# Performance work log

Measured on AMD Instinct MI355X. Metric: run time of the kernel, lower is better.

Reference implementation:

```python
import jax, jax.numpy as jnp
import numpy as np

B, S, D = 2, 2048, 2048
H, KV, DK = 16, 4, 128
G = H // KV  # GQA groups
EPS = 1e-6
BASE = 10000.0


def _rope_tables(seq_len, dim):
    inv_freq = 1.0 / (BASE ** (jnp.arange(0, dim, 2, dtype=jnp.float32) / dim))
    t = jnp.arange(seq_len, dtype=jnp.float32)
    freqs = t[:, None] * inv_freq[None, :]            # [S, dim/2]
    emb = jnp.concatenate([freqs, freqs], axis=-1)    # [S, dim]
    # broadcast over [b, s, h, d]
    return jnp.cos(emb)[None, :, None, :], jnp.sin(emb)[None, :, None, :]


def _rotate_half(x):
    x1, x2 = jnp.split(x, 2, axis=-1)
    return jnp.concatenate([-x2, x1], axis=-1)


def _rms_norm(x, w):
    return x * jax.lax.rsqrt(jnp.mean(x * x, axis=-1, keepdims=True) + EPS) * w


def setup_inputs() -> dict:
    key = jax.random.key(0)
    ks = jax.random.split(key, 5)
    std = 0.02
    return {
        "x": jax.random.normal(ks[0], (B, S, D), jnp.float32),
        "Wq": jax.random.normal(ks[1], (D, H * DK), jnp.float32) * std,
        "Wk": jax.random.normal(ks[2], (D, KV * DK), jnp.float32) * std,
        "Wv": jax.random.normal(ks[3], (D, KV * DK), jnp.float32) * std,
        "Wo": jax.random.normal(ks[4], (H * DK, D), jnp.float32) * std,
        "q_norm_w": jnp.ones((DK,), jnp.float32),
        "k_norm_w": jnp.ones((DK,), jnp.float32),
    }


def reference(x, Wq, Wk, Wv, Wo, q_norm_w, k_norm_w):
    b, s, d = x.shape
    q = (x @ Wq).reshape(b, s, H, DK)
    k = (x @ Wk).reshape(b, s, KV, DK)
    v = (x @ Wv).reshape(b, s, KV, DK)

    # per-head RMSNorm on q/k
    q = _rms_norm(q, q_norm_w)
    k = _rms_norm(k, k_norm_w)

    # RoPE (applied in [b, s, h, d] layout like the original)
    cos, sin = _rope_tables(s, DK)
    q = q * cos + _rotate_half(q) * sin
    k = k * cos + _rotate_half(k) * sin

    # GQA attention without materializing repeated K/V:
    # q: [b, kv, g, s, d];  k, v: [b, kv, s, d]
    q = q.transpose(0, 2, 1, 3).reshape(b, KV, G, s, DK)
    k = k.transpose(0, 2, 1, 3)
    v = v.transpose(0, 2, 1, 3)

    scale = 1.0 / np.sqrt(DK)
    scores = jnp.einsum('bkgqd,bkpd->bkgqp', q, k) * scale  # [b,kv,g,s,s]
    causal = jnp.tril(jnp.ones((s, s), dtype=bool))
    scores = jnp.where(causal, scores, jnp.finfo(scores.dtype).min)
    attn = jax.nn.softmax(scores, axis=-1)
    out = jnp.einsum('bkgqp,bkpd->bkgqd', attn, v)           # [b,kv,g,s,d]

    out = out.reshape(b, H, s, DK).transpose(0, 2, 1, 3).reshape(b, s, H * DK)
    return out @ Wo
```

## Files before the change

kernel.cpp:

```cpp
#include <hip/hip_runtime.h>

typedef __attribute__((ext_vector_type(4))) float f32x4;
typedef __attribute__((ext_vector_type(8))) short s16x8;

struct alignas(8) us4 { ushort x, y, z, w; };

__device__ __forceinline__ ushort f2bf(float f) {
  unsigned u = __builtin_bit_cast(unsigned, f);
  u += 0x7fffu + ((u >> 16) & 1u);
  return (ushort)(u >> 16);
}
__device__ __forceinline__ float bf2f(ushort h) {
  unsigned u = ((unsigned)h) << 16;
  return __builtin_bit_cast(float, u);
}

__device__ __forceinline__ void gload_lds16(const ushort* g, ushort* l) {
  __builtin_amdgcn_global_load_lds((const __attribute__((address_space(1))) unsigned int*)g,
                                   (__attribute__((address_space(3))) unsigned int*)l, 16, 0, 0);
}

__global__ __launch_bounds__(256) void preproc_kernel(
    const float* __restrict__ x, const float* __restrict__ Wq, const float* __restrict__ Wk,
    const float* __restrict__ Wv, const float* __restrict__ Wo,
    ushort* __restrict__ xb, ushort* __restrict__ WqkvT, ushort* __restrict__ WoT,
    float* __restrict__ rc, float* __restrict__ rs) {
  __shared__ float tile[32][33];
  int bid = blockIdx.x, tid = threadIdx.x;
  if (bid < 2048) {
    const int n4 = 4096 * 2048 / 4;
    for (int i = bid * 256 + tid; i < n4; i += 2048 * 256) {
      float4 v = reinterpret_cast<const float4*>(x)[i];
      us4 o;
      o.x = f2bf(v.x); o.y = f2bf(v.y); o.z = f2bf(v.z); o.w = f2bf(v.w);
      reinterpret_cast<us4*>(xb)[i] = o;
    }
  } else if (bid < 2560) {
    int t = (bid - 2048) * 4 + (tid >> 6), j = tid & 63;
    float inv = expf(-(float)j * (9.210340371976184f / 64.0f));
    float ang = (float)t * inv;
    float s, c;
    sincosf(ang, &s, &c);
    rc[t * 64 + j] = c;
    rs[t * 64 + j] = s;
  } else {
    int wid = bid - 2560;
    const float* src;
    ushort* dst;
    int C, bx, by;
    if (wid < 4096) { src = Wq; dst = WqkvT; C = 2048; bx = wid & 63; by = wid >> 6; }
    else if (wid < 5120) { int w2 = wid - 4096; src = Wk; dst = WqkvT + (size_t)2048 * 2048; C = 512; bx = w2 & 15; by = w2 >> 4; }
    else if (wid < 6144) { int w2 = wid - 5120; src = Wv; dst = WqkvT + (size_t)2560 * 2048; C = 512; bx = w2 & 15; by = w2 >> 4; }
    else { int w2 = wid - 6144; src = Wo; dst = WoT; C = 2048; bx = w2 & 63; by = w2 >> 6; }
    int c0 = bx * 32, r0 = by * 32;
    int tx = tid & 31, ty = tid >> 5;
#pragma unroll
    for (int i = 0; i < 4; ++i)
      tile[ty + i * 8][tx] = src[(size_t)(r0 + ty + i * 8) * C + c0 + tx];
    __syncthreads();
#pragma unroll
    for (int i = 0; i < 4; ++i)
      dst[(size_t)(c0 + ty + i * 8) * 2048 + r0 + tx] = f2bf(tile[tx][ty + i * 8]);
  }
}

__global__ __launch_bounds__(256) void postqkv_kernel(
    const ushort* __restrict__ qkv, const float* __restrict__ kw,
    ushort* __restrict__ Kb, ushort* __restrict__ vt,
    const float* __restrict__ rc, const float* __restrict__ rs) {
  __shared__ ushort tile[64][136];
  int bid = blockIdx.x, tid = threadIdx.x;
  if (bid < 4096) {
    int wv = tid >> 6, lane = tid & 63;
    int row = bid * 4 + wv;
    int token = row >> 2, head = row & 3;
    const ushort* p = qkv + (size_t)token * 3072 + 2048 + head * 128;
    float x1 = bf2f(p[lane]), x2 = bf2f(p[lane + 64]);
    float ss = x1 * x1 + x2 * x2;
#pragma unroll
    for (int m = 32; m > 0; m >>= 1) ss += __shfl_xor(ss, m);
    float r = rsqrtf(ss * (1.0f / 128.0f) + 1e-6f);
    float xn1 = x1 * r * kw[lane], xn2 = x2 * r * kw[lane + 64];
    int t = token & 2047;
    float c = rc[t * 64 + lane], s = rs[t * 64 + lane];
    ushort* o = Kb + (size_t)token * 512 + head * 128;
    o[lane] = f2bf(xn1 * c - xn2 * s);
    o[lane + 64] = f2bf(xn2 * c + xn1 * s);
  } else {
    int bx = bid - 4096;
    int st = bx & 31, kvh = (bx >> 5) & 3, b = bx >> 7;
    int s0 = st * 64;
#pragma unroll
    for (int p = 0; p < 4; ++p) {
      int idx = p * 2048 + tid * 8;
      int s = idx >> 7, d = idx & 127;
      *(s16x8*)&tile[s][d] =
          *(const s16x8*)&qkv[(size_t)(b * 2048 + s0 + s) * 3072 + 2560 + kvh * 128 + d];
    }
    __syncthreads();
#pragma unroll
    for (int p = 0; p < 4; ++p) {
      int idx = p * 2048 + tid * 8;
      int d = idx >> 6, s = idx & 63;
      s16x8 v;
#pragma unroll
      for (int u = 0; u < 8; ++u) v[u] = (short)tile[s + u][d];
      *(s16x8*)&vt[(size_t)((b * 4 + kvh) * 128 + d) * 2048 + s0 + s] = v;
    }
  }
}

template <bool OUTF32>
__global__ __launch_bounds__(512, 2) void gemm256_kernel(const ushort* __restrict__ A,
                                                         const ushort* __restrict__ Bt,
                                                         void* __restrict__ Cp,
                                                         int M, int N, int K) {
  __shared__ ushort As[3][256][64];
  __shared__ ushort Bs[3][128][64];
  int tid = threadIdx.x;
  int lane = tid & 63, wv = tid >> 6;
  int wm = wv >> 1, wn = wv & 1;
  int lr = lane & 15, lg = lane >> 4;
  int nwg = gridDim.x * gridDim.y;
  int flat = blockIdx.y * gridDim.x + blockIdx.x;
  int swz = (flat & 7) * (nwg >> 3) + (flat >> 3);
  int bx = swz % gridDim.x, by = swz / gridDim.x;
  int m0 = by * 256, n0 = bx * 128;
  int srow8 = lane >> 3;
  int gcol = ((lane & 7) * 8) ^ (srow8 << 3);
  int nt = K >> 6;

  const ushort* Abase = A + (size_t)m0 * K;
  const ushort* Bbase = Bt + (size_t)n0 * K;

  auto stageA = [&](int slot, int t, int p) {
    int r0 = (wv * 4 + p) * 8;
    gload_lds16(&Abase[(size_t)(r0 + srow8) * K + t * 64 + gcol], &As[slot][r0][0]);
  };
  auto stageB = [&](int slot, int t, int p) {
    int r0 = (wv * 2 + p) * 8;
    gload_lds16(&Bbase[(size_t)(r0 + srow8) * K + t * 64 + gcol], &Bs[slot][r0][0]);
  };

  stageA(0, 0, 0); stageA(0, 0, 1); stageB(0, 0, 0);
  stageA(0, 0, 2); stageA(0, 0, 3); stageB(0, 0, 1);
  stageA(1, 1, 0); stageA(1, 1, 1); stageB(1, 1, 0);
  stageA(1, 1, 2); stageA(1, 1, 3); stageB(1, 1, 1);

  f32x4 acc[4][4] = {};
  int arow[4], brow[4], aswz[4], bswz[4];
#pragma unroll
  for (int i = 0; i < 4; ++i) {
    arow[i] = wm * 64 + i * 16 + lr;
    aswz[i] = (arow[i] & 7) << 3;
    brow[i] = wn * 64 + i * 16 + lr;
    bswz[i] = (brow[i] & 7) << 3;
  }

  for (int t = 0; t < nt; ++t) {
    int cur = t % 3, pf = (t + 2) % 3;
    if (t + 1 < nt) {
      asm volatile("s_waitcnt vmcnt(6)" ::: "memory");
    } else {
      asm volatile("s_waitcnt vmcnt(0)" ::: "memory");
    }
    __builtin_amdgcn_s_barrier();
    bool do_pf = (t + 2) < nt;
    {
      s16x8 a[4], b[4];
#pragma unroll
      for (int i = 0; i < 4; ++i) a[i] = *(const s16x8*)&As[cur][arow[i]][(lg * 8) ^ aswz[i]];
#pragma unroll
      for (int j = 0; j < 4; ++j) b[j] = *(const s16x8*)&Bs[cur][brow[j]][(lg * 8) ^ bswz[j]];
      if (do_pf) { stageA(pf, t + 2, 0); stageA(pf, t + 2, 1); stageB(pf, t + 2, 0); }
      __builtin_amdgcn_s_setprio(1);
#pragma unroll
      for (int i = 0; i < 4; ++i)
#pragma unroll
        for (int j = 0; j < 4; ++j)
          acc[i][j] = __builtin_amdgcn_mfma_f32_16x16x32_bf16(a[i], b[j], acc[i][j], 0, 0, 0);
      __builtin_amdgcn_s_setprio(0);
    }
    {
      s16x8 a[4], b[4];
#pragma unroll
      for (int i = 0; i < 4; ++i) a[i] = *(const s16x8*)&As[cur][arow[i]][(32 + lg * 8) ^ aswz[i]];
#pragma unroll
      for (int j = 0; j < 4; ++j) b[j] = *(const s16x8*)&Bs[cur][brow[j]][(32 + lg * 8) ^ bswz[j]];
      if (do_pf) { stageA(pf, t + 2, 2); stageA(pf, t + 2, 3); stageB(pf, t + 2, 1); }
      __builtin_amdgcn_s_setprio(1);
#pragma unroll
      for (int i = 0; i < 4; ++i)
#pragma unroll
        for (int j = 0; j < 4; ++j)
          acc[i][j] = __builtin_amdgcn_mfma_f32_16x16x32_bf16(a[i], b[j], acc[i][j], 0, 0, 0);
      __builtin_amdgcn_s_setprio(0);
    }
  }
#pragma unroll
  for (int i = 0; i < 4; ++i)
#pragma unroll
    for (int j = 0; j < 4; ++j) {
      int row = m0 + wm * 64 + i * 16 + lg * 4;
      int col = n0 + wn * 64 + j * 16 + lr;
#pragma unroll
      for (int r = 0; r < 4; ++r) {
        float v = acc[i][j][r];
        if (OUTF32)
          reinterpret_cast<float*>(Cp)[(size_t)(row + r) * N + col] = v;
        else
          reinterpret_cast<ushort*>(Cp)[(size_t)(row + r) * N + col] = f2bf(v);
      }
    }
}

__global__ __launch_bounds__(256, 2) void attn_kernel(const ushort* __restrict__ QKV,
                                                      const ushort* __restrict__ Kn,
                                                      const ushort* __restrict__ Vt,
                                                      ushort* __restrict__ AO,
                                                      const float* __restrict__ rc,
                                                      const float* __restrict__ rs,
                                                      const float* __restrict__ qw) {
  __shared__ ushort Ks[2][64][128];
  __shared__ ushort Vs[2][128][64];
  __shared__ ushort Ps[4][32][64];
  int bxi = blockIdx.x;
  int g = bxi >> 5, bh = bxi & 31;
  int qt = (g < 8) ? (15 - g) : (g - 8);
  int b = bh >> 4, h = bh & 15, kvh = h >> 2;
  int q0 = qt * 128;
  int nt = 2 * qt + 2;
  int tid = threadIdx.x, lane = tid & 63, w = tid >> 6;
  int lr = lane & 15, lg = lane >> 4;

  int ksrow = lane >> 4, kscol = (lane & 15) * 8;
  int vsrow = lane >> 3, vscol = (lane & 7) * 8;

  auto stage = [&](int c, int t) {
    int p0 = t * 64;
#pragma unroll
    for (int p = 0; p < 4; ++p) {
      int r0 = w * 16 + p * 4;
      int row = r0 + ksrow;
      int gc = kscol ^ ((row & 7) << 3);
      gload_lds16(&Kn[(size_t)(b * 2048 + p0 + row) * 512 + kvh * 128 + gc], &Ks[c][r0][0]);
    }
#pragma unroll
    for (int p = 0; p < 4; ++p) {
      int r0 = w * 32 + p * 8;
      int row = r0 + vsrow;
      int gc = vscol ^ ((row & 7) << 3);
      gload_lds16(&Vt[(size_t)((b * 4 + kvh) * 128 + row) * 2048 + p0 + gc], &Vs[c][r0][0]);
    }
  };

  stage(0, 0);

  const float QSCALE = 0.12751744f;
  s16x8 qf[2][4];
#pragma unroll
  for (int qa = 0; qa < 2; ++qa) {
    int t_tok = q0 + w * 32 + qa * 16 + lr;
    const ushort* qp = QKV + (size_t)(b * 2048 + t_tok) * 3072 + h * 128;
    float xv[4][8];
    float ss = 0.f;
#pragma unroll
    for (int ks = 0; ks < 4; ++ks) {
      s16x8 raw = *(const s16x8*)&qp[ks * 32 + lg * 8];
#pragma unroll
      for (int j = 0; j < 8; ++j) {
        float x = bf2f((ushort)raw[j]);
        xv[ks][j] = x;
        ss += x * x;
      }
    }
    ss += __shfl_xor(ss, 16);
    ss += __shfl_xor(ss, 32);
    float rms = rsqrtf(ss * (1.0f / 128.0f) + 1e-6f);
#pragma unroll
    for (int ks = 0; ks < 2; ++ks) {
      int dbase = ks * 32 + lg * 8;
      float cc[8], sn[8], w1[8], w2[8];
      *(float4*)&cc[0] = *(const float4*)&rc[(size_t)t_tok * 64 + dbase];
      *(float4*)&cc[4] = *(const float4*)&rc[(size_t)t_tok * 64 + dbase + 4];
      *(float4*)&sn[0] = *(const float4*)&rs[(size_t)t_tok * 64 + dbase];
      *(float4*)&sn[4] = *(const float4*)&rs[(size_t)t_tok * 64 + dbase + 4];
      *(float4*)&w1[0] = *(const float4*)&qw[dbase];
      *(float4*)&w1[4] = *(const float4*)&qw[dbase + 4];
      *(float4*)&w2[0] = *(const float4*)&qw[dbase + 64];
      *(float4*)&w2[4] = *(const float4*)&qw[dbase + 68];
      s16x8 o1, o2;
#pragma unroll
      for (int j = 0; j < 8; ++j) {
        float x1 = xv[ks][j] * rms * w1[j];
        float x2 = xv[ks + 2][j] * rms * w2[j];
        o1[j] = (short)f2bf((x1 * cc[j] - x2 * sn[j]) * QSCALE);
        o2[j] = (short)f2bf((x2 * cc[j] + x1 * sn[j]) * QSCALE);
      }
      qf[qa][ks] = o1;
      qf[qa][ks + 2] = o2;
    }
  }

  f32x4 O[2][8] = {};
  float mrow[2] = {-1e30f, -1e30f};
  float lrow[2] = {0.f, 0.f};

  for (int t = 0; t < nt; ++t) {
    int c = t & 1;
    if (t + 1 < nt) {
      stage(c ^ 1, t + 1);
      asm volatile("s_waitcnt vmcnt(8)" ::: "memory");
    } else {
      asm volatile("s_waitcnt vmcnt(0)" ::: "memory");
    }
    __builtin_amdgcn_s_barrier();

    bool skip = (t == 2 * qt + 1) && (w < 2);
    if (!skip) {
      f32x4 sacc[2][4] = {};
      __builtin_amdgcn_s_setprio(1);
#pragma unroll
      for (int ks = 0; ks < 4; ++ks) {
        s16x8 bk[4];
#pragma unroll
        for (int fp = 0; fp < 4; ++fp) {
          int kr = fp * 16 + lr;
          bk[fp] = *(const s16x8*)&Ks[c][kr][(ks * 32 + lg * 8) ^ ((kr & 7) << 3)];
        }
#pragma unroll
        for (int qa = 0; qa < 2; ++qa)
#pragma unroll
          for (int fp = 0; fp < 4; ++fp)
            sacc[qa][fp] = __builtin_amdgcn_mfma_f32_16x16x32_bf16(bk[fp], qf[qa][ks], sacc[qa][fp], 0, 0, 0);
      }
      __builtin_amdgcn_s_setprio(0);

      if (t >= 2 * qt) {
        int p0 = t * 64;
#pragma unroll
        for (int qa = 0; qa < 2; ++qa)
#pragma unroll
          for (int fp = 0; fp < 4; ++fp)
#pragma unroll
            for (int r = 0; r < 4; ++r) {
              int qg = q0 + w * 32 + qa * 16 + lr;
              int pg = p0 + fp * 16 + lg * 4 + r;
              if (pg > qg) sacc[qa][fp][r] = -1e30f;
            }
      }

      float pml[2];
#pragma unroll
      for (int qa = 0; qa < 2; ++qa) {
        float m0 = fmaxf(fmaxf(sacc[qa][0][0], sacc[qa][0][1]), fmaxf(sacc[qa][0][2], sacc[qa][0][3]));
        float m1 = fmaxf(fmaxf(sacc[qa][1][0], sacc[qa][1][1]), fmaxf(sacc[qa][1][2], sacc[qa][1][3]));
        float m2 = fmaxf(fmaxf(sacc[qa][2][0], sacc[qa][2][1]), fmaxf(sacc[qa][2][2], sacc[qa][2][3]));
        float m3 = fmaxf(fmaxf(sacc[qa][3][0], sacc[qa][3][1]), fmaxf(sacc[qa][3][2], sacc[qa][3][3]));
        pml[qa] = fmaxf(fmaxf(m0, m1), fmaxf(m2, m3));
      }
      bool need = (pml[0] > mrow[0] + 8.0f) | (pml[1] > mrow[1] + 8.0f);
      if (__any((int)need)) {
        float fsc[2];
#pragma unroll
        for (int qa = 0; qa < 2; ++qa) {
          float pm = fmaxf(pml[qa], __shfl_xor(pml[qa], 16));
          pm = fmaxf(pm, __shfl_xor(pm, 32));
          float mn = fmaxf(mrow[qa], pm);
          fsc[qa] = __builtin_amdgcn_exp2f(mrow[qa] - mn);
          mrow[qa] = mn;
          lrow[qa] *= fsc[qa];
        }
#pragma unroll
        for (int qa = 0; qa < 2; ++qa) {
          float fo[4];
#pragma unroll
          for (int r = 0; r < 4; ++r) fo[r] = __shfl(fsc[qa], lg * 4 + r);
#pragma unroll
          for (int fn = 0; fn < 8; ++fn)
#pragma unroll
            for (int r = 0; r < 4; ++r) O[qa][fn][r] *= fo[r];
        }
      }
#pragma unroll
      for (int qa = 0; qa < 2; ++qa) {
        float ls = 0.f;
        int prow = qa * 16 + lr;
        int swz = (lr & 7) << 3;
#pragma unroll
        for (int fp = 0; fp < 4; ++fp) {
          float e0 = __builtin_amdgcn_exp2f(sacc[qa][fp][0] - mrow[qa]);
          float e1 = __builtin_amdgcn_exp2f(sacc[qa][fp][1] - mrow[qa]);
          float e2 = __builtin_amdgcn_exp2f(sacc[qa][fp][2] - mrow[qa]);
          float e3 = __builtin_amdgcn_exp2f(sacc[qa][fp][3] - mrow[qa]);
          ls += (e0 + e1) + (e2 + e3);
          unsigned lo = (unsigned)f2bf(e0) | ((unsigned)f2bf(e1) << 16);
          unsigned hi = (unsigned)f2bf(e2) | ((unsigned)f2bf(e3) << 16);
          uint2 pk; pk.x = lo; pk.y = hi;
          *reinterpret_cast<uint2*>(&Ps[w][prow][(fp * 16 + lg * 4) ^ swz]) = pk;
        }
        lrow[qa] += ls;
      }
      __builtin_amdgcn_s_setprio(1);
#pragma unroll
      for (int ks2 = 0; ks2 < 2; ++ks2) {
        s16x8 ap[2];
#pragma unroll
        for (int qa = 0; qa < 2; ++qa) {
          int prow = qa * 16 + lr;
          ap[qa] = *(const s16x8*)&Ps[w][prow][(ks2 * 32 + lg * 8) ^ ((lr & 7) << 3)];
        }
#pragma unroll
        for (int fn = 0; fn < 8; ++fn) {
          int vrow = fn * 16 + lr;
          s16x8 bv = *(const s16x8*)&Vs[c][vrow][(ks2 * 32 + lg * 8) ^ ((vrow & 7) << 3)];
#pragma unroll
          for (int qa = 0; qa < 2; ++qa)
            O[qa][fn] = __builtin_amdgcn_mfma_f32_16x16x32_bf16(ap[qa], bv, O[qa][fn], 0, 0, 0);
        }
      }
      __builtin_amdgcn_s_setprio(0);
    }
    __builtin_amdgcn_s_barrier();
  }

#pragma unroll
  for (int qa = 0; qa < 2; ++qa) {
    lrow[qa] += __shfl_xor(lrow[qa], 16);
    lrow[qa] += __shfl_xor(lrow[qa], 32);
  }
#pragma unroll
  for (int qa = 0; qa < 2; ++qa) {
    float inv = 1.0f / lrow[qa];
    float invq[4];
#pragma unroll
    for (int r = 0; r < 4; ++r) invq[r] = __shfl(inv, lg * 4 + r);
#pragma unroll
    for (int fn = 0; fn < 8; ++fn)
#pragma unroll
      for (int r = 0; r < 4; ++r) {
        size_t idx = (size_t)(b * 2048 + q0 + w * 32 + qa * 16 + lg * 4 + r) * 2048 +
                     h * 128 + fn * 16 + lr;
        AO[idx] = f2bf(O[qa][fn][r] * invq[r]);
      }
  }
}

extern "C" void kernel_launch(void* const* d_in, const int* in_sizes, int n_in,
                              void* d_out, int out_size, void* d_ws, size_t ws_size,
                              hipStream_t stream) {
  (void)in_sizes; (void)n_in; (void)out_size; (void)ws_size;
  const float* x = (const float*)d_in[0];
  const float* Wq = (const float*)d_in[1];
  const float* Wk = (const float*)d_in[2];
  const float* Wv = (const float*)d_in[3];
  const float* Wo = (const float*)d_in[4];
  const float* qw = (const float*)d_in[5];
  const float* kw = (const float*)d_in[6];
  float* out = (float*)d_out;

  char* ws = (char*)d_ws;
  size_t off = 0;
  auto alloc = [&](size_t bytes) {
    void* p = ws + off;
    off += (bytes + 255) & ~(size_t)255;
    return p;
  };
  ushort* xb = (ushort*)alloc((size_t)4096 * 2048 * 2);
  ushort* WqkvT = (ushort*)alloc((size_t)3072 * 2048 * 2);
  ushort* WoT = (ushort*)alloc((size_t)2048 * 2048 * 2);
  ushort* QKVraw = (ushort*)alloc((size_t)4096 * 3072 * 2);
  ushort* Kb = (ushort*)alloc((size_t)4096 * 512 * 2);
  ushort* Vt = (ushort*)alloc((size_t)4096 * 512 * 2);
  ushort* AO = (ushort*)alloc((size_t)4096 * 2048 * 2);
  float* rc = (float*)alloc((size_t)2048 * 64 * 4);
  float* rs = (float*)alloc((size_t)2048 * 64 * 4);

  preproc_kernel<<<12800, 256, 0, stream>>>(x, Wq, Wk, Wv, Wo, xb, WqkvT, WoT, rc, rs);
  gemm256_kernel<false><<<dim3(24, 16), 512, 0, stream>>>(xb, WqkvT, QKVraw, 4096, 3072, 2048);
  postqkv_kernel<<<4352, 256, 0, stream>>>(QKVraw, kw, Kb, Vt, rc, rs);
  attn_kernel<<<512, 256, 0, stream>>>(QKVraw, Kb, Vt, AO, rc, rs, qw);
  gemm256_kernel<true><<<dim3(16, 16), 512, 0, stream>>>(AO, WoT, out, 4096, 2048, 2048);
}
```

Before: 198.5 us.

## Split long causal attention tiles into two KV chunks with a merge kernel

Query tiles 8-15 of the causal attention are now split into two KV-range chunks, handled by separate blocks, which raises the grid from 512 to 768 blocks and evens out per-block work. Each chunk writes unnormalized bf16 partial outputs plus row max and sum, and a new merge kernel combines them with log-sum-exp rescaling into the attention output. The aim is to cut the load imbalance tail of the triangular workload. In exchange it adds an extra kernel launch, extra global traffic for the partials, and a bf16 rounding of the partial outputs.

```diff
diff --git a/kernel.cpp b/kernel.cpp
--- a/kernel.cpp
+++ b/kernel.cpp
@@ -214,22 +214,29 @@
     }
 }
 
+__device__ const int QT_TAB[24] = {15,15,7,14,14,13,13,6,12,12,11,11,5,10,10,9,9,4,8,8,3,2,1,0};
+__device__ const int CK_TAB[24] = { 0, 1,-1, 0, 1, 0, 1,-1, 0, 1, 0, 1,-1, 0, 1, 0, 1,-1, 0, 1,-1,-1,-1,-1};
+
 __global__ __launch_bounds__(256, 2) void attn_kernel(const ushort* __restrict__ QKV,
                                                       const ushort* __restrict__ Kn,
                                                       const ushort* __restrict__ Vt,
                                                       ushort* __restrict__ AO,
                                                       const float* __restrict__ rc,
                                                       const float* __restrict__ rs,
-                                                      const float* __restrict__ qw) {
+                                                      const float* __restrict__ qw,
+                                                      ushort* __restrict__ PO,
+                                                      float2* __restrict__ ML) {
   __shared__ ushort Ks[2][64][128];
   __shared__ ushort Vs[2][128][64];
   __shared__ ushort Ps[4][32][64];
   int bxi = blockIdx.x;
-  int g = bxi >> 5, bh = bxi & 31;
-  int qt = (g < 8) ? (15 - g) : (g - 8);
+  int cls = bxi >> 5, bh = bxi & 31;
+  int qt = QT_TAB[cls], ck = CK_TAB[cls];
   int b = bh >> 4, h = bh & 15, kvh = h >> 2;
   int q0 = qt * 128;
   int nt = 2 * qt + 2;
+  int t0 = (ck == 1) ? (qt + 1) : 0;
+  int tend = (ck == 0) ? (qt + 1) : nt;
   int tid = threadIdx.x, lane = tid & 63, w = tid >> 6;
   int lr = lane & 15, lg = lane >> 4;
 
@@ -254,7 +261,7 @@
     }
   };
 
-  stage(0, 0);
+  stage(t0 & 1, t0);
 
   const float QSCALE = 0.12751744f;
   s16x8 qf[2][4];
@@ -306,9 +313,9 @@
   float mrow[2] = {-1e30f, -1e30f};
   float lrow[2] = {0.f, 0.f};
 
-  for (int t = 0; t < nt; ++t) {
+  for (int t = t0; t < tend; ++t) {
     int c = t & 1;
-    if (t + 1 < nt) {
+    if (t + 1 < tend) {
       stage(c ^ 1, t + 1);
       asm volatile("s_waitcnt vmcnt(8)" ::: "memory");
     } else {
@@ -429,20 +436,67 @@
     lrow[qa] += __shfl_xor(lrow[qa], 16);
     lrow[qa] += __shfl_xor(lrow[qa], 32);
   }
-#pragma unroll
-  for (int qa = 0; qa < 2; ++qa) {
-    float inv = 1.0f / lrow[qa];
-    float invq[4];
-#pragma unroll
-    for (int r = 0; r < 4; ++r) invq[r] = __shfl(inv, lg * 4 + r);
-#pragma unroll
-    for (int fn = 0; fn < 8; ++fn)
-#pragma unroll
-      for (int r = 0; r < 4; ++r) {
-        size_t idx = (size_t)(b * 2048 + q0 + w * 32 + qa * 16 + lg * 4 + r) * 2048 +
-                     h * 128 + fn * 16 + lr;
-        AO[idx] = f2bf(O[qa][fn][r] * invq[r]);
-      }
+
+  if (ck < 0) {
+#pragma unroll
+    for (int qa = 0; qa < 2; ++qa) {
+      float inv = 1.0f / lrow[qa];
+      float invq[4];
+#pragma unroll
+      for (int r = 0; r < 4; ++r) invq[r] = __shfl(inv, lg * 4 + r);
+#pragma unroll
+      for (int fn = 0; fn < 8; ++fn)
+#pragma unroll
+        for (int r = 0; r < 4; ++r) {
+          size_t idx = (size_t)(b * 2048 + q0 + w * 32 + qa * 16 + lg * 4 + r) * 2048 +
+                       h * 128 + fn * 16 + lr;
+          AO[idx] = f2bf(O[qa][fn][r] * invq[r]);
+        }
+    }
+  } else {
+    const size_t CS = (size_t)2 * 16 * 1024 * 128;
+#pragma unroll
+    for (int qa = 0; qa < 2; ++qa) {
+#pragma unroll
+      for (int fn = 0; fn < 8; ++fn)
+#pragma unroll
+        for (int r = 0; r < 4; ++r) {
+          int q = q0 + w * 32 + qa * 16 + lg * 4 + r;
+          size_t idx = (size_t)ck * CS +
+                       ((size_t)(b * 16 + h) * 1024 + (q - 1024)) * 128 + fn * 16 + lr;
+          PO[idx] = f2bf(O[qa][fn][r]);
+        }
+      if (lg == 0) {
+        int qrow = q0 + w * 32 + qa * 16 + lr;
+        ML[(size_t)ck * 65536 + (size_t)(b * 16 + h) * 1024 + (qrow - 1024)] =
+            make_float2(mrow[qa], lrow[qa]);
+      }
+    }
+  }
+}
+
+__global__ __launch_bounds__(256) void attn_merge_kernel(const ushort* __restrict__ PO,
+                                                         const float2* __restrict__ ML,
+                                                         ushort* __restrict__ AO) {
+  const size_t CS = (size_t)2 * 16 * 1024 * 128;
+  int wid = blockIdx.x * 4 + (threadIdx.x >> 6);
+  int lane = threadIdx.x & 63;
+  for (int rid = wid; rid < 32768; rid += 8192) {
+    int b = rid >> 14, h = (rid >> 10) & 15, qi = rid & 1023;
+    float2 mla = ML[(size_t)(b * 16 + h) * 1024 + qi];
+    float2 mlb = ML[65536 + (size_t)(b * 16 + h) * 1024 + qi];
+    float m = fmaxf(mla.x, mlb.x);
+    float fa = __builtin_amdgcn_exp2f(mla.x - m);
+    float fb = __builtin_amdgcn_exp2f(mlb.x - m);
+    float inv = 1.0f / (fa * mla.y + fb * mlb.y);
+    size_t base = ((size_t)(b * 16 + h) * 1024 + qi) * 128 + lane * 2;
+    ushort2 oa = *reinterpret_cast<const ushort2*>(&PO[base]);
+    ushort2 ob = *reinterpret_cast<const ushort2*>(&PO[CS + base]);
+    ushort2 o;
+    o.x = f2bf((fa * bf2f(oa.x) + fb * bf2f(ob.x)) * inv);
+    o.y = f2bf((fa * bf2f(oa.y) + fb * bf2f(ob.y)) * inv);
+    size_t ao = (size_t)(b * 2048 + 1024 + qi) * 2048 + h * 128 + lane * 2;
+    *reinterpret_cast<ushort2*>(&AO[ao]) = o;
   }
 }
 
@@ -475,10 +529,13 @@
   ushort* AO = (ushort*)alloc((size_t)4096 * 2048 * 2);
   float* rc = (float*)alloc((size_t)2048 * 64 * 4);
   float* rs = (float*)alloc((size_t)2048 * 64 * 4);
+  ushort* PO = (ushort*)alloc((size_t)2 * 2 * 16 * 1024 * 128 * 2);
+  float2* ML = (float2*)alloc((size_t)2 * 65536 * 8);
 
   preproc_kernel<<<12800, 256, 0, stream>>>(x, Wq, Wk, Wv, Wo, xb, WqkvT, WoT, rc, rs);
   gemm256_kernel<false><<<dim3(24, 16), 512, 0, stream>>>(xb, WqkvT, QKVraw, 4096, 3072, 2048);
   postqkv_kernel<<<4352, 256, 0, stream>>>(QKVraw, kw, Kb, Vt, rc, rs);
-  attn_kernel<<<512, 256, 0, stream>>>(QKVraw, Kb, Vt, AO, rc, rs, qw);
+  attn_kernel<<<768, 256, 0, stream>>>(QKVraw, Kb, Vt, AO, rc, rs, qw, PO, ML);
+  attn_merge_kernel<<<2048, 256, 0, stream>>>(PO, ML, AO);
   gemm256_kernel<true><<<dim3(16, 16), 512, 0, stream>>>(AO, WoT, out, 4096, 2048, 2048);
 }
```

Result: no change. 202.0 us (+1.8%).

## Use 256x256 tile GEMM kernel for fused QKV projection

Applied to the files above, without the earlier changes.

Adds a new GEMM kernel with 256x256 output tiles, a 2x4 wave layout and double-buffered LDS staging, and uses it for the QKV projection instead of the 256x128 triple-buffered kernel. Larger tiles raise arithmetic intensity per LDS load and halve the block count to 192, fewer than the CU count. The cost is one block per CU, reduced occupancy, shallower pipelining, and some idle CUs on MI355X's 256 CUs.

```diff
diff --git a/kernel.cpp b/kernel.cpp
--- a/kernel.cpp
+++ b/kernel.cpp
@@ -111,6 +111,102 @@
 }
 
 template <bool OUTF32>
+__global__ __launch_bounds__(512, 1) void gemm256sq_kernel(const ushort* __restrict__ A,
+                                                           const ushort* __restrict__ Bt,
+                                                           void* __restrict__ Cp,
+                                                           int M, int N, int K) {
+  __shared__ ushort As[2][256][64];
+  __shared__ ushort Bs[2][256][64];
+  int tid = threadIdx.x;
+  int lane = tid & 63, wv = tid >> 6;
+  int wm = wv >> 2, wn = wv & 3;
+  int lr = lane & 15, lg = lane >> 4;
+  int nwg = gridDim.x * gridDim.y;
+  int flat = blockIdx.y * gridDim.x + blockIdx.x;
+  int swz = (flat & 7) * (nwg >> 3) + (flat >> 3);
+  int bx = swz % gridDim.x, by = swz / gridDim.x;
+  int m0 = by * 256, n0 = bx * 256;
+  int srow8 = lane >> 3;
+  int gcol = ((lane & 7) * 8) ^ (srow8 << 3);
+  int nt = K >> 6;
+
+  const ushort* Abase = A + (size_t)m0 * K;
+  const ushort* Bbase = Bt + (size_t)n0 * K;
+
+  auto stage = [&](int slot, int t) {
+#pragma unroll
+    for (int p = 0; p < 4; ++p) {
+      int r0 = wv * 32 + p * 8;
+      gload_lds16(&Abase[(size_t)(r0 + srow8) * K + t * 64 + gcol], &As[slot][r0][0]);
+    }
+#pragma unroll
+    for (int p = 0; p < 4; ++p) {
+      int r0 = wv * 32 + p * 8;
+      gload_lds16(&Bbase[(size_t)(r0 + srow8) * K + t * 64 + gcol], &Bs[slot][r0][0]);
+    }
+  };
+
+  stage(0, 0);
+
+  f32x4 acc[8][4] = {};
+  int arow[8], aswz[8], brow[4], bswz[4];
+#pragma unroll
+  for (int i = 0; i < 8; ++i) {
+    arow[i] = wm * 128 + i * 16 + lr;
+    aswz[i] = (arow[i] & 7) << 3;
+  }
+#pragma unroll
+  for (int j = 0; j < 4; ++j) {
+    brow[j] = wn * 64 + j * 16 + lr;
+    bswz[j] = (brow[j] & 7) << 3;
+  }
+
+  for (int t = 0; t < nt; ++t) {
+    int c = t & 1;
+    if (t + 1 < nt) {
+      stage(c ^ 1, t + 1);
+      asm volatile("s_waitcnt vmcnt(8)" ::: "memory");
+    } else {
+      asm volatile("s_waitcnt vmcnt(0)" ::: "memory");
+    }
+    __builtin_amdgcn_s_barrier();
+#pragma unroll
+    for (int ks = 0; ks < 2; ++ks) {
+      s16x8 a[8], b[4];
+#pragma unroll
+      for (int i = 0; i < 8; ++i)
+        a[i] = *(const s16x8*)&As[c][arow[i]][(ks * 32 + lg * 8) ^ aswz[i]];
+#pragma unroll
+      for (int j = 0; j < 4; ++j)
+        b[j] = *(const s16x8*)&Bs[c][brow[j]][(ks * 32 + lg * 8) ^ bswz[j]];
+      __builtin_amdgcn_s_setprio(1);
+#pragma unroll
+      for (int i = 0; i < 8; ++i)
+#pragma unroll
+        for (int j = 0; j < 4; ++j)
+          acc[i][j] = __builtin_amdgcn_mfma_f32_16x16x32_bf16(a[i], b[j], acc[i][j], 0, 0, 0);
+      __builtin_amdgcn_s_setprio(0);
+    }
+    __builtin_amdgcn_s_barrier();
+  }
+#pragma unroll
+  for (int i = 0; i < 8; ++i)
+#pragma unroll
+    for (int j = 0; j < 4; ++j) {
+      int row = m0 + wm * 128 + i * 16 + lg * 4;
+      int col = n0 + wn * 64 + j * 16 + lr;
+#pragma unroll
+      for (int r = 0; r < 4; ++r) {
+        float v = acc[i][j][r];
+        if (OUTF32)
+          reinterpret_cast<float*>(Cp)[(size_t)(row + r) * N + col] = v;
+        else
+          reinterpret_cast<ushort*>(Cp)[(size_t)(row + r) * N + col] = f2bf(v);
+      }
+    }
+}
+
+template <bool OUTF32>
 __global__ __launch_bounds__(512, 2) void gemm256_kernel(const ushort* __restrict__ A,
                                                          const ushort* __restrict__ Bt,
                                                          void* __restrict__ Cp,
@@ -477,7 +573,7 @@
   float* rs = (float*)alloc((size_t)2048 * 64 * 4);
 
   preproc_kernel<<<12800, 256, 0, stream>>>(x, Wq, Wk, Wv, Wo, xb, WqkvT, WoT, rc, rs);
-  gemm256_kernel<false><<<dim3(24, 16), 512, 0, stream>>>(xb, WqkvT, QKVraw, 4096, 3072, 2048);
+  gemm256sq_kernel<false><<<dim3(12, 16), 512, 0, stream>>>(xb, WqkvT, QKVraw, 4096, 3072, 2048);
   postqkv_kernel<<<4352, 256, 0, stream>>>(QKVraw, kw, Kb, Vt, rc, rs);
   attn_kernel<<<512, 256, 0, stream>>>(QKVraw, Kb, Vt, AO, rc, rs, qw);
   gemm256_kernel<true><<<dim3(16, 16), 512, 0, stream>>>(AO, WoT, out, 4096, 2048, 2048);
```

After: 198.9 us. About the same (+0.2%).

## Feed softmax probabilities directly from registers into 16x16x16 MFMA for PV

Applied to the files above, without the earlier changes.

Instead of writing the exponentiated scores to a per-wave LDS buffer and reading them back in the 16x16x32 A-operand layout, the PV product now uses the 16x16x16 bf16 MFMA. Its A-operand layout matches the QK accumulator output, so probabilities go straight from registers. This removes the LDS round trip and the Ps buffer, which may help occupancy. The cost is twice as many MFMA instructions and narrower 8-byte V loads from LDS.

```diff
diff --git a/kernel.cpp b/kernel.cpp
--- a/kernel.cpp
+++ b/kernel.cpp
@@ -2,8 +2,19 @@
 
 typedef __attribute__((ext_vector_type(4))) float f32x4;
 typedef __attribute__((ext_vector_type(8))) short s16x8;
+typedef __attribute__((ext_vector_type(4))) short s16x4;
 
 struct alignas(8) us4 { ushort x, y, z, w; };
+
+#if __has_builtin(__builtin_amdgcn_mfma_f32_16x16x16bf16_1k)
+#define MFMA16(a, b, c) __builtin_amdgcn_mfma_f32_16x16x16bf16_1k(a, b, c, 0, 0, 0)
+#define HAVE_MFMA16 1
+#elif __has_builtin(__builtin_amdgcn_mfma_f32_16x16x16_bf16)
+#define MFMA16(a, b, c) __builtin_amdgcn_mfma_f32_16x16x16_bf16(a, b, c, 0, 0, 0)
+#define HAVE_MFMA16 1
+#else
+#define HAVE_MFMA16 0
+#endif
 
 __device__ __forceinline__ ushort f2bf(float f) {
   unsigned u = __builtin_bit_cast(unsigned, f);
@@ -223,7 +234,9 @@
                                                       const float* __restrict__ qw) {
   __shared__ ushort Ks[2][64][128];
   __shared__ ushort Vs[2][128][64];
+#if !HAVE_MFMA16
   __shared__ ushort Ps[4][32][64];
+#endif
   int bxi = blockIdx.x;
   int g = bxi >> 5, bh = bxi & 31;
   int qt = (g < 8) ? (15 - g) : (g - 8);
@@ -382,6 +395,41 @@
             for (int r = 0; r < 4; ++r) O[qa][fn][r] *= fo[r];
         }
       }
+#if HAVE_MFMA16
+      s16x4 pa[2][4];
+#pragma unroll
+      for (int qa = 0; qa < 2; ++qa) {
+        float ls = 0.f;
+#pragma unroll
+        for (int fp = 0; fp < 4; ++fp) {
+          float e0 = __builtin_amdgcn_exp2f(sacc[qa][fp][0] - mrow[qa]);
+          float e1 = __builtin_amdgcn_exp2f(sacc[qa][fp][1] - mrow[qa]);
+          float e2 = __builtin_amdgcn_exp2f(sacc[qa][fp][2] - mrow[qa]);
+          float e3 = __builtin_amdgcn_exp2f(sacc[qa][fp][3] - mrow[qa]);
+          ls += (e0 + e1) + (e2 + e3);
+          s16x4 pk;
+          pk[0] = (short)f2bf(e0);
+          pk[1] = (short)f2bf(e1);
+          pk[2] = (short)f2bf(e2);
+          pk[3] = (short)f2bf(e3);
+          pa[qa][fp] = pk;
+        }
+        lrow[qa] += ls;
+      }
+      __builtin_amdgcn_s_setprio(1);
+#pragma unroll
+      for (int kc = 0; kc < 4; ++kc) {
+#pragma unroll
+        for (int fn = 0; fn < 8; ++fn) {
+          int vrow = fn * 16 + lr;
+          s16x4 bv = *(const s16x4*)&Vs[c][vrow][(kc * 16 + lg * 4) ^ ((vrow & 7) << 3)];
+#pragma unroll
+          for (int qa = 0; qa < 2; ++qa)
+            O[qa][fn] = MFMA16(pa[qa][kc], bv, O[qa][fn]);
+        }
+      }
+      __builtin_amdgcn_s_setprio(0);
+#else
 #pragma unroll
       for (int qa = 0; qa < 2; ++qa) {
         float ls = 0.f;
@@ -420,6 +468,7 @@
         }
       }
       __builtin_amdgcn_s_setprio(0);
+#endif
     }
     __builtin_amdgcn_s_barrier();
   }
```

New measurement: 207.8 us. 1.05x slower.
